# Optimization experiments

Measured on AMD Instinct MI355X. Metric: run time of the kernel, lower is better.

## Reference

```python
import jax, jax.numpy as jnp
import numpy as np

V = 64                 # |Sigma|
IN_DIM = V + 2         # Sigma + '(' + ')'
OUT_DIM = V + 1        # Sigma + <del>/<end>
H = 512
B = 256
SX = 34                # max proto length 32 + 2 boundaries
SY = 34
BIG_NEG = -1000000000.0


def _one_hot_seq(key, S, batch):
    # '(' at pos 0, L random symbols, ')' at pos L+1, zero padding after
    kl, ks = jax.random.split(key)
    lengths = jax.random.randint(kl, (batch,), 4, S - 1)        # L in [4, S-2]
    syms = jax.random.randint(ks, (S, batch), 0, V)
    pos = jnp.arange(S)[:, None]
    tok = jnp.where(pos == 0, V, jnp.where(pos == lengths[None, :] + 1, V + 1, syms))
    oh = jax.nn.one_hot(tok, IN_DIM, dtype=jnp.float32)
    valid = (pos <= lengths[None, :] + 1).astype(jnp.float32)
    return oh * valid[:, :, None]


def setup_inputs() -> dict:
    key = jax.random.key(0)
    ks = jax.random.split(key, 14)

    def p(k, shape, scale):
        return jax.random.uniform(k, shape, jnp.float32, -scale, scale)

    s = 1.0 / float(np.sqrt(H))
    s2 = 1.0 / float(np.sqrt(2 * H))
    return {
        "sources": _one_hot_seq(ks[0], SX, B),
        "targets": _one_hot_seq(ks[1], SY, B),
        # bidirectional prior LSTM (input IN_DIM -> hidden H, fwd + rev)
        "Wih_f": p(ks[2], (4 * H, IN_DIM), s), "Whh_f": p(ks[3], (4 * H, H), s), "b_f": p(ks[4], (4 * H,), s),
        "Wih_r": p(ks[5], (4 * H, IN_DIM), s), "Whh_r": p(ks[6], (4 * H, H), s), "b_r": p(ks[7], (4 * H,), s),
        # modern LSTM (input IN_DIM -> hidden 2H)
        "Wih_m": p(ks[8], (8 * H, IN_DIM), s2), "Whh_m": p(ks[9], (8 * H, 2 * H), s2), "b_m": p(ks[10], (8 * H,), s2),
        # heads: Linear(2H -> OUT_DIM) + LogSoftmax
        "W_sub": p(ks[11], (OUT_DIM, 2 * H), s2), "b_sub": jnp.zeros((OUT_DIM,), jnp.float32),
        "W_ins": p(ks[12], (OUT_DIM, 2 * H), s2), "b_ins": jnp.zeros((OUT_DIM,), jnp.float32),
    }


def _lstm(x, Wih, Whh, b, hid):
    # torch gate order: i, f, g, o
    bsz = x.shape[1]
    def step(carry, xt):
        h, c = carry
        g = xt @ Wih.T + h @ Whh.T + b
        i, f, gg, o = jnp.split(g, 4, axis=-1)
        c = jax.nn.sigmoid(f) * c + jax.nn.sigmoid(i) * jnp.tanh(gg)
        h = jax.nn.sigmoid(o) * jnp.tanh(c)
        return (h, c), h
    init = (jnp.zeros((bsz, hid), x.dtype), jnp.zeros((bsz, hid), x.dtype))
    _, hs = jax.lax.scan(step, init, x)
    return hs  # [S, B, hid]


def _forward(sources, targets, Wih_f, Whh_f, b_f, Wih_r, Whh_r, b_r,
             Wih_m, Whh_m, b_m, W_sub, b_sub, W_ins, b_ins):
    x_fwd = _lstm(sources, Wih_f, Whh_f, b_f, H)
    x_bwd = _lstm(sources[::-1], Wih_r, Whh_r, b_r, H)[::-1]
    x_emb = jnp.concatenate([x_fwd, x_bwd], axis=-1)   # [SX, B, 2H]
    y_emb = _lstm(targets, Wih_m, Whh_m, b_m, 2 * H)    # [SY, B, 2H]

    # head(x_emb[i] + y_emb[j]) decomposes since Linear is affine
    def pair_logprobs(W, bb):
        lx = jnp.einsum('ibh,oh->ibo', x_emb, W)              # [SX, B, O]
        ly = jnp.einsum('jbh,oh->jbo', y_emb, W) + bb         # [SY, B, O]
        return jax.nn.log_softmax(lx[:, None] + ly[None, :], axis=-1)  # [SX, SY, B, O]

    sub_log = pair_logprobs(W_sub, b_sub)
    ins_log = pair_logprobs(W_ins, b_ins)

    # cell (i, j, b) is computed iff x[i] and y[j] are real (non-padding) one-hots, j <= max_cognat_length
    x_any = sources.sum(-1) > 0                                # [SX, B]
    y_any = targets.sum(-1) > 0                                # [SY, B]
    j_ok = jnp.arange(SY) < SY - 1
    valid = x_any[:, None, :] & (y_any & j_ok[:, None])[None, :, :]   # [SX, SY, B]

    end = jnp.where(valid, ins_log[..., V], BIG_NEG)           # insProbs[V_SIZE]
    dlt = jnp.where(valid, sub_log[..., V], BIG_NEG)           # subProbs[V_SIZE]

    y_next = jnp.pad(targets[1:], ((0, 1), (0, 0), (0, 0)))    # y[j+1], [SY, B, IN_DIM]
    ins_ok = valid & (y_next[..., IN_DIM - 1] == 0)[None]      # not bool(y[j+1, V_SIZE+1])
    ins_val = jnp.einsum('ijbv,jbv->ijb', ins_log[..., :V], y_next[..., :V])
    sub_val = jnp.einsum('ijbv,jbv->ijb', sub_log[..., :V], y_next[..., :V])

    # stacked cached probs: [ins, sub, end, del], each [SX, SY, B]
    return jnp.stack([
        jnp.where(ins_ok, ins_val, BIG_NEG),
        jnp.where(ins_ok, sub_val, BIG_NEG),
        end,
        dlt,
    ])


def reference(sources, targets, Wih_f, Whh_f, b_f, Wih_r, Whh_r, b_r,
              Wih_m, Whh_m, b_m, W_sub, b_sub, W_ins, b_ins):
    return _forward(sources, targets, Wih_f, Whh_f, b_f, Wih_r, Whh_r, b_r,
                    Wih_m, Whh_m, b_m, W_sub, b_sub, W_ins, b_ins)
```

## Files before the change

### kernel.cpp

```cpp
#include <hip/hip_runtime.h>

typedef __attribute__((ext_vector_type(4))) float f32x4;
typedef unsigned char u8;
typedef unsigned long long u64t;

#define BIG_NEG -1000000000.0f

static constexpr int B_  = 256;
static constexpr int SX_ = 34;
static constexpr int SY_ = 34;
static constexpr int IND = 66;
static constexpr int OP_ = 80;

__device__ __forceinline__ f32x4 mfma_fp8(long a, long b, f32x4 c) {
  return __builtin_amdgcn_mfma_f32_16x16x32_fp8_fp8(a, b, c, 0, 0, 0);
}
__device__ __forceinline__ float sigm(float x)  { return 1.0f / (1.0f + __expf(-x)); }
__device__ __forceinline__ float tanhx(float x) { return 2.0f * sigm(2.0f * x) - 1.0f; }
template <bool HI>
__device__ __forceinline__ unsigned pk2(float a, float b, unsigned old) {
  return __builtin_amdgcn_cvt_pk_fp8_f32(a, b, (int)old, HI);
}

__global__ void decode_tokens(const float* __restrict__ src,
                              const float* __restrict__ tgt,
                              int* __restrict__ tok_x, int* __restrict__ tok_y) {
  int idx = blockIdx.x * 256 + threadIdx.x;
  const int half = SX_ * B_;
  if (idx >= 2 * half) return;
  const float* base = (idx < half) ? src : tgt;
  int* outp         = (idx < half) ? tok_x : tok_y;
  int k = (idx < half) ? idx : idx - half;
  const float* p = base + (size_t)k * IND;
  int tok = -1;
  for (int v = 0; v < IND; ++v) if (p[v] > 0.5f) tok = v;
  outp[k] = tok;
}

__global__ void conv_fp8_all(const float* __restrict__ Wf, const float* __restrict__ Wr,
                             const float* __restrict__ Wm,
                             u8* __restrict__ of, u8* __restrict__ orr, u8* __restrict__ om) {
  const int F4 = 2048 * 512 / 4;
  const int M4 = 4096 * 1024 / 4;
  int i = blockIdx.x * 256 + threadIdx.x;
  int stride = gridDim.x * 256;
  for (; i < 2 * F4 + M4; i += stride) {
    const float* src; unsigned* dst; int k;
    if (i < F4)          { src = Wf; dst = (unsigned*)of;  k = i; }
    else if (i < 2 * F4) { src = Wr; dst = (unsigned*)orr; k = i - F4; }
    else                 { src = Wm; dst = (unsigned*)om;  k = i - 2 * F4; }
    float4 f = ((const float4*)src)[k];
    unsigned w = pk2<false>(f.x, f.y, 0);
    w = pk2<true>(f.z, f.w, w);
    dst[k] = w;
  }
}

__global__ __launch_bounds__(256) void build_E_all(
    const float* __restrict__ Wf, const float* __restrict__ bf,
    const float* __restrict__ Wr, const float* __restrict__ br,
    const float* __restrict__ Wm, const float* __restrict__ bm,
    float* __restrict__ Ef, float* __restrict__ Er, float* __restrict__ Em) {
  __shared__ float tile[64 * 67];
  int tb = blockIdx.x;
  const float* W; const float* bias; float* E; int H4; int n0;
  if (tb < 32)      { W = Wf; bias = bf; E = Ef; H4 = 2048; n0 = tb * 64; }
  else if (tb < 64) { W = Wr; bias = br; E = Er; H4 = 2048; n0 = (tb - 32) * 64; }
  else              { W = Wm; bias = bm; E = Em; H4 = 4096; n0 = (tb - 64) * 64; }
  const float* src = W + (size_t)n0 * IND;
  for (int i = threadIdx.x; i < 64 * IND; i += 256) {
    int n = i / IND, v = i - n * IND;
    tile[n * 67 + v] = src[i];
  }
  __syncthreads();
  int lane = threadIdx.x & 63, w = threadIdx.x >> 6;
  float bl = bias[n0 + lane];
  for (int v = w; v < 67; v += 4) {
    float val = (v < 66 ? tile[lane * 67 + v] : 0.f) + bl;
    E[(size_t)v * H4 + n0 + lane] = val;
  }
}

__global__ void pad_head_w(const float* __restrict__ Wsub, const float* __restrict__ Wins,
                           u8* __restrict__ Wcat) {
  int widx = blockIdx.x * 256 + threadIdx.x;
  if (widx >= 160 * 256) return;
  int row = widx >> 8;
  int wc  = widx & 255;
  int srow = row < 80 ? row : row - 80;
  const float* W = row < 80 ? Wsub : Wins;
  float f0 = 0.f, f1 = 0.f, f2 = 0.f, f3 = 0.f;
  if (srow < 65) {
    const float* p = W + (size_t)srow * 1024 + wc * 4;
    f0 = p[0]; f1 = p[1]; f2 = p[2]; f3 = p[3];
  }
  unsigned w = pk2<false>(f0, f1, 0);
  w = pk2<true>(f2, f3, w);
  ((unsigned*)Wcat)[widx] = w;
}

template <int HH, int NS>
__device__ __forceinline__ void run_lstm(
    const u8* __restrict__ w8, const float* __restrict__ E,
    bool revr, u8* __restrict__ hall, int b0, int h0,
    unsigned* __restrict__ flags, int dom0, int myid,
    u8* __restrict__ alds, u8* __restrict__ hT, const u8* __restrict__ tok_small) {
  const int tid = threadIdx.x;
  const int lane = tid & 63, w = tid >> 6;
  const int lo = lane & 15, q = lane >> 4;
  constexpr int AST = HH + 8;
  constexpr int U8C = HH / 8;
  constexpr int USH = (HH == 1024) ? 7 : 6;
  constexpr int NI  = (32 * U8C) / 256;
  constexpr int NK  = HH / 32;
  const int hh = lo & 7;
  const bool hi = (lo >= 8);
  const int hu_e = h0 + w * 8 + hh;

  long breg0[NK], breg1[NK];
  {
    const u8* brow0 = w8 + (size_t)((lo >> 3) * HH + hu_e) * HH + q * 8;
    const u8* brow1 = w8 + (size_t)((2 + (lo >> 3)) * HH + hu_e) * HH + q * 8;
#pragma unroll
    for (int kk = 0; kk < NK; ++kk) {
      breg0[kk] = *(const long*)(brow0 + kk * 32);
      breg1[kk] = *(const long*)(brow1 + kk * 32);
    }
  }
  float creg[4] = {0.f, 0.f, 0.f, 0.f};

  for (int t = 0; t < 34; ++t) {
    const u8* hsrc = hall + (size_t)t * (256 * HH);
    u64t tmp[NI];
#pragma unroll
    for (int ii = 0; ii < NI; ++ii) {
      int idx = tid + ii * 256;
      tmp[ii] = __hip_atomic_load(
          (const u64t*)(hsrc + (size_t)(b0 + (idx >> USH)) * HH + (idx & (U8C - 1)) * 8),
          __ATOMIC_RELAXED, __HIP_MEMORY_SCOPE_AGENT);
    }
#pragma unroll
    for (int ii = 0; ii < NI; ++ii) {
      int idx = tid + ii * 256;
      *(u64t*)&alds[(idx >> USH) * AST + (idx & (U8C - 1)) * 8] = tmp[ii];
    }
    __syncthreads();

    f32x4 acc[2][2];
#pragma unroll
    for (int mt = 0; mt < 2; ++mt) {
      acc[mt][0] = (f32x4){0.f, 0.f, 0.f, 0.f};
      acc[mt][1] = (f32x4){0.f, 0.f, 0.f, 0.f};
    }
    const u8* a0p = alds + lo * AST + q * 8;
    const u8* a1p = alds + (16 + lo) * AST + q * 8;
#pragma unroll
    for (int kk = 0; kk < NK; ++kk) {
      long a0 = *(const long*)(a0p + kk * 32);
      long a1 = *(const long*)(a1p + kk * 32);
      acc[0][0] = mfma_fp8(a0, breg0[kk], acc[0][0]);
      acc[0][1] = mfma_fp8(a0, breg1[kk], acc[0][1]);
      acc[1][0] = mfma_fp8(a1, breg0[kk], acc[1][0]);
      acc[1][1] = mfma_fp8(a1, breg1[kk], acc[1][1]);
    }

    int tpos = revr ? 33 - t : t;
    const u8* tkp = tok_small + tpos * 32;
#pragma unroll
    for (int mt = 0; mt < 2; ++mt) {
      f32x4 t0 = acc[mt][0], t1 = acc[mt][1];
      f32x4 p0, p1;
#pragma unroll
      for (int c2 = 0; c2 < 4; ++c2) {
        p0[c2] = __shfl_xor(t0[c2], 8, 64);
        p1[c2] = __shfl_xor(t1[c2], 8, 64);
      }
#pragma unroll
      for (int rr = 0; rr < 2; ++rr) {
        int r = (hi ? 2 : 0) + rr;
        float iv = hi ? p0[r] : t0[r];
        float fv = hi ? t0[r] : p0[r];
        float gv = hi ? p1[r] : t1[r];
        float ov = hi ? t1[r] : p1[r];
        int m = mt * 16 + q * 4 + r;
        int v = tkp[m];
        const float* e = E + (size_t)v * (4 * HH) + hu_e;
        iv += e[0]; fv += e[HH]; gv += e[2 * HH]; ov += e[3 * HH];
        float cold = creg[mt * 2 + rr];
        float cn = sigm(fv) * cold + sigm(iv) * tanhx(gv);
        float hn = sigm(ov) * tanhx(cn);
        creg[mt * 2 + rr] = cn;
        hT[m * 32 + w * 8 + hh] = (u8)(pk2<false>(hn, hn, 0) & 0xffu);
      }
    }
    __syncthreads();

    {
      int m = tid >> 3, cc = tid & 7;
      unsigned val = *(const unsigned*)&hT[m * 32 + cc * 4];
      u8* hdst = hall + (size_t)(t + 1) * (256 * HH);
      __hip_atomic_store((unsigned*)(hdst + (size_t)(b0 + m) * HH + h0 + cc * 4),
                         val, __ATOMIC_RELAXED, __HIP_MEMORY_SCOPE_AGENT);
    }

    if (t < 33) {
      __asm__ volatile("s_waitcnt vmcnt(0)" ::: "memory");
      __syncthreads();
      unsigned tgt = (unsigned)(t + 1);
      if (tid == 0)
        __hip_atomic_store(&flags[(dom0 + myid) * 32], tgt,
                           __ATOMIC_RELAXED, __HIP_MEMORY_SCOPE_AGENT);
      if (tid < NS) {
        int spin = 0;
        for (;;) {
          unsigned v = __hip_atomic_load(&flags[(dom0 + tid) * 32],
                                         __ATOMIC_RELAXED, __HIP_MEMORY_SCOPE_AGENT);
          if (__ballot(v < tgt) == 0) break;
          __builtin_amdgcn_s_sleep(1);
          if (++spin > (1 << 17)) break;
        }
      }
      __syncthreads();
    }
  }
}

__global__ __launch_bounds__(256, 2) void lstm_persist(
    const int* __restrict__ tok_x, const int* __restrict__ tok_y,
    const float* __restrict__ E_f, const u8* __restrict__ w8_f,
    const float* __restrict__ E_r, const u8* __restrict__ w8_r,
    const float* __restrict__ E_m, const u8* __restrict__ w8_m,
    u8* __restrict__ fwd_all, u8* __restrict__ rev_all, u8* __restrict__ y_all,
    unsigned* __restrict__ flags) {
  __shared__ u8 alds[32 * 1032];
  __shared__ u8 hT[32 * 32];
  __shared__ u8 tok_small[34 * 32];

  const int b = blockIdx.x;
  int role, c, s;
  if (b < 256)      { role = 2; c = b >> 5; s = b & 31; }
  else if (b < 384) { int l = b - 256; role = 0; c = l >> 4; s = l & 15; }
  else              { int l = b - 384; role = 1; c = l >> 4; s = l & 15; }

  const float* E  = role == 0 ? E_f  : role == 1 ? E_r  : E_m;
  const u8*    w8 = role == 0 ? w8_f : role == 1 ? w8_r : w8_m;
  u8* hall        = role == 0 ? fwd_all : role == 1 ? rev_all : y_all;
  const int* tokg = (role == 2) ? tok_y : tok_x;
  const int b0 = c * 32;
  const int h0 = s * 32;
  const int dom0 = (role == 2) ? c * 32 : (role == 0) ? 256 + c * 16 : 384 + c * 16;

  for (int i = threadIdx.x; i < 34 * 32; i += 256) {
    int t2 = i >> 5, m = i & 31;
    int tk = tokg[t2 * 256 + b0 + m];
    tok_small[i] = (u8)(tk < 0 ? 66 : tk);
  }
  __syncthreads();

  if (role == 2)
    run_lstm<1024, 32>(w8, E, false, hall, b0, h0, flags, dom0, s, alds, hT, tok_small);
  else
    run_lstm<512, 16>(w8, E, role == 1, hall, b0, h0, flags, dom0, s, alds, hT, tok_small);
}

__global__ __launch_bounds__(256, 1) void head_kernel(
    const u8* __restrict__ fwd_all, const u8* __restrict__ rev_all,
    const u8* __restrict__ y_all, const u8* __restrict__ Wcat,
    const float* __restrict__ b_sub, const float* __restrict__ b_ins,
    float* __restrict__ lx_sub, float* __restrict__ lx_ins,
    float* __restrict__ ly_sub, float* __restrict__ ly_ins) {
  __shared__ u8 wq[160 * 264];
  const int lane = threadIdx.x & 63, wave = threadIdx.x >> 6;
  const int lo = lane & 15, q = lane >> 4;
  int blk = blockIdx.x;
  bool yside = (blk >= 68);
  int mb = yside ? blk - 68 : blk;
  int ij = mb >> 1;
  int bbase = (mb & 1) * 128;

  f32x4 acc[2][10];
#pragma unroll
  for (int mt = 0; mt < 2; ++mt)
#pragma unroll
    for (int nn = 0; nn < 10; ++nn) acc[mt][nn] = (f32x4){0.f,0.f,0.f,0.f};

  for (int qk = 0; qk < 4; ++qk) {
    long aA[2][8];
#pragma unroll
    for (int mt = 0; mt < 2; ++mt) {
      int row = bbase + wave * 32 + mt * 16 + lo;
      const u8* ab;
      if (yside)
        ab = y_all + ((size_t)(ij + 1) * 256 + row) * 1024 + qk * 256 + q * 8;
      else if (qk < 2)
        ab = fwd_all + ((size_t)(ij + 1) * 256 + row) * 512 + qk * 256 + q * 8;
      else
        ab = rev_all + ((size_t)(34 - ij) * 256 + row) * 512 + (qk - 2) * 256 + q * 8;
#pragma unroll
      for (int ki = 0; ki < 8; ++ki) aA[mt][ki] = *(const long*)(ab + ki * 32);
    }

    for (int c8 = threadIdx.x; c8 < 160 * 32; c8 += 256) {
      int row = c8 >> 5, col = (c8 & 31) << 3;
      *(long*)&wq[row * 264 + col] =
          *(const long*)&Wcat[(size_t)row * 1024 + qk * 256 + col];
    }
    __syncthreads();

#pragma unroll
    for (int ki = 0; ki < 8; ++ki) {
#pragma unroll
      for (int nn = 0; nn < 10; ++nn) {
        long bf = *(const long*)&wq[(nn * 16 + lo) * 264 + ki * 32 + q * 8];
        acc[0][nn] = mfma_fp8(aA[0][ki], bf, acc[0][nn]);
        acc[1][nn] = mfma_fp8(aA[1][ki], bf, acc[1][nn]);
      }
    }
    __syncthreads();
  }

#pragma unroll
  for (int mt = 0; mt < 2; ++mt) {
#pragma unroll
    for (int nn = 0; nn < 10; ++nn) {
      bool is_sub = (nn < 5);
      int n = (is_sub ? nn : nn - 5) * 16 + lo;
      float bias = 0.0f;
      if (yside && n < 65) bias = is_sub ? b_sub[n] : b_ins[n];
      float* dst = yside ? (is_sub ? ly_sub : ly_ins) : (is_sub ? lx_sub : lx_ins);
#pragma unroll
      for (int r = 0; r < 4; ++r) {
        int b = bbase + wave * 32 + mt * 16 + q * 4 + r;
        dst[((size_t)ij * 256 + b) * OP_ + n] = acc[mt][nn][r] + bias;
      }
    }
  }
}

__device__ __forceinline__ void lse_regs(const float4* __restrict__ X,
                                         const float* __restrict__ py, int sym,
                                         float& logZ, float& v64, float& vs) {
  const float4* py4 = (const float4*)py;
  float4 Y[17];
#pragma unroll
  for (int q = 0; q < 17; ++q) Y[q] = py4[q];
  float mm = -3.4e38f;
#pragma unroll
  for (int q = 0; q < 17; ++q) {
    float vx[4] = {X[q].x + Y[q].x, X[q].y + Y[q].y, X[q].z + Y[q].z, X[q].w + Y[q].w};
#pragma unroll
    for (int c = 0; c < 4; ++c) {
      int o = q * 4 + c;
      if (o < 65) mm = fmaxf(mm, vx[c]);
    }
  }
  float ss = 0.f, vsl = 0.f, vend = 0.f;
#pragma unroll
  for (int q = 0; q < 17; ++q) {
    float vx[4] = {X[q].x + Y[q].x, X[q].y + Y[q].y, X[q].z + Y[q].z, X[q].w + Y[q].w};
#pragma unroll
    for (int c = 0; c < 4; ++c) {
      int o = q * 4 + c;
      if (o < 65) {
        ss += __expf(vx[c] - mm);
        if (o == 64) vend = vx[c];
        if (o == sym) vsl = vx[c];
      }
    }
  }
  logZ = mm + __logf(ss);
  v64 = vend;
  vs = vsl;
}

__global__ __launch_bounds__(256, 1) void pair_kernel(
    const int* __restrict__ tok_x, const int* __restrict__ tok_y,
    const float* __restrict__ lx_sub, const float* __restrict__ lx_ins,
    const float* __restrict__ ly_sub, const float* __restrict__ ly_ins,
    float* __restrict__ out) {
  const int i = blockIdx.x >> 2;
  const int bc = blockIdx.x & 3;
  const int jq = threadIdx.x >> 6;
  const int bl = threadIdx.x & 63;
  const int b = bc * 64 + bl;
  const size_t CH = (size_t)SX_ * SY_ * B_;

  float4 Xs[17], Xi[17];
  {
    const float4* ps = (const float4*)(lx_sub + ((size_t)i * 256 + b) * OP_);
    const float4* pi = (const float4*)(lx_ins + ((size_t)i * 256 + b) * OP_);
#pragma unroll
    for (int q = 0; q < 17; ++q) { Xs[q] = ps[q]; Xi[q] = pi[q]; }
  }
  int tx = tok_x[i * 256 + b];

  for (int j = jq; j < 34; j += 4) {
    size_t obase = ((size_t)i * SY_ + j) * 256 + b;
    bool dead = (j == SY_ - 1) || (tx < 0);
    if (!dead) {
      int ty = tok_y[j * 256 + b];
      if (ty < 0) dead = true;
    }
    if (dead) {
      out[obase] = BIG_NEG;
      out[CH + obase] = BIG_NEG;
      out[2 * CH + obase] = BIG_NEG;
      out[3 * CH + obase] = BIG_NEG;
      continue;
    }
    int tn = tok_y[(j + 1) * 256 + b];
    bool ins_ok = (tn != 65);
    int sym = (tn >= 0 && tn < 64) ? tn : -1;

    float logZs, v64s, vss;
    lse_regs(Xs, ly_sub + ((size_t)j * 256 + b) * OP_, sym, logZs, v64s, vss);
    float dlt = v64s - logZs;
    float sub_val = (sym >= 0) ? (vss - logZs) : 0.0f;

    float logZi, v64i, vsi;
    lse_regs(Xi, ly_ins + ((size_t)j * 256 + b) * OP_, sym, logZi, v64i, vsi);
    float endv = v64i - logZi;
    float ins_val = (sym >= 0) ? (vsi - logZi) : 0.0f;

    out[obase]          = ins_ok ? ins_val : BIG_NEG;
    out[CH + obase]     = ins_ok ? sub_val : BIG_NEG;
    out[2 * CH + obase] = endv;
    out[3 * CH + obase] = dlt;
  }
}

extern "C" void kernel_launch(void* const* d_in, const int* in_sizes, int n_in,
                              void* d_out, int out_size, void* d_ws, size_t ws_size,
                              hipStream_t stream) {
  const float* sources = (const float*)d_in[0];
  const float* targets = (const float*)d_in[1];
  const float* Wih_f = (const float*)d_in[2];
  const float* Whh_f = (const float*)d_in[3];
  const float* b_f   = (const float*)d_in[4];
  const float* Wih_r = (const float*)d_in[5];
  const float* Whh_r = (const float*)d_in[6];
  const float* b_r   = (const float*)d_in[7];
  const float* Wih_m = (const float*)d_in[8];
  const float* Whh_m = (const float*)d_in[9];
  const float* b_m   = (const float*)d_in[10];
  const float* W_sub = (const float*)d_in[11];
  const float* b_sub = (const float*)d_in[12];
  const float* W_ins = (const float*)d_in[13];
  const float* b_ins = (const float*)d_in[14];
  float* out = (float*)d_out;

  char* w = (char*)d_ws;
  constexpr size_t FLAG_SZ = 512 * 32 * 4;
  constexpr size_t TOK_SZ  = (size_t)SX_ * B_ * 4;
  constexpr size_t WCAT_SZ = (size_t)160 * 1024;
  constexpr size_t W8F_SZ  = (size_t)2048 * 512;
  constexpr size_t W8M_SZ  = (size_t)4096 * 1024;
  constexpr size_t EF_SZ   = (size_t)67 * 2048 * 4;
  constexpr size_t EM_SZ   = (size_t)67 * 4096 * 4;
  constexpr size_t LX_SZ   = (size_t)SX_ * B_ * OP_ * 4;
  constexpr size_t HF_SZ   = (size_t)35 * B_ * 512;
  constexpr size_t HM_SZ   = (size_t)35 * B_ * 1024;

  size_t off = 0;
  unsigned* flags = (unsigned*)(w + off); off += FLAG_SZ;
  int*  tok_x   = (int*)(w + off);  off += TOK_SZ;
  int*  tok_y   = (int*)(w + off);  off += TOK_SZ;
  off = (off + 255) & ~(size_t)255;
  u8*   Wcat    = (u8*)(w + off);   off += WCAT_SZ;
  u8*   w8_f    = (u8*)(w + off);   off += W8F_SZ;
  u8*   w8_r    = (u8*)(w + off);   off += W8F_SZ;
  u8*   w8_m    = (u8*)(w + off);   off += W8M_SZ;
  float* E_f    = (float*)(w + off); off += EF_SZ;
  float* E_r    = (float*)(w + off); off += EF_SZ;
  float* E_m    = (float*)(w + off); off += EM_SZ;
  float* lx_sub = (float*)(w + off); off += LX_SZ;
  float* lx_ins = (float*)(w + off); off += LX_SZ;
  float* ly_sub = (float*)(w + off); off += LX_SZ;
  float* ly_ins = (float*)(w + off); off += LX_SZ;
  u8* fwd_all   = (u8*)(w + off);   off += HF_SZ;
  u8* rev_all   = (u8*)(w + off);   off += HF_SZ;
  u8* y_all     = (u8*)(w + off);   off += HM_SZ;
  (void)ws_size; (void)in_sizes; (void)n_in; (void)out_size;

  (void)hipMemsetAsync(flags, 0, FLAG_SZ, stream);
  (void)hipMemsetAsync(fwd_all, 0, (size_t)B_ * 512, stream);
  (void)hipMemsetAsync(rev_all, 0, (size_t)B_ * 512, stream);
  (void)hipMemsetAsync(y_all,   0, (size_t)B_ * 1024, stream);

  decode_tokens<<<(2 * SX_ * B_ + 255) / 256, 256, 0, stream>>>(sources, targets, tok_x, tok_y);
  pad_head_w<<<160, 256, 0, stream>>>(W_sub, W_ins, Wcat);
  conv_fp8_all<<<3072, 256, 0, stream>>>(Whh_f, Whh_r, Whh_m, w8_f, w8_r, w8_m);
  build_E_all<<<128, 256, 0, stream>>>(Wih_f, b_f, Wih_r, b_r, Wih_m, b_m, E_f, E_r, E_m);

  lstm_persist<<<512, 256, 0, stream>>>(
      tok_x, tok_y,
      E_f, w8_f,
      E_r, w8_r,
      E_m, w8_m,
      fwd_all, rev_all, y_all, flags);

  head_kernel<<<136, 256, 0, stream>>>(fwd_all, rev_all, y_all, Wcat,
                                       b_sub, b_ins, lx_sub, lx_ins, ly_sub, ly_ins);

  pair_kernel<<<136, 256, 0, stream>>>(tok_x, tok_y, lx_sub, lx_ins,
                                       ly_sub, ly_ins, out);
}
```

Baseline: 370.6 us.

## Fuse prep kernels, skip zero-state step, double head/pair grid parallelism

Merges the four preprocessing kernels into one prep_all launch with block-range dispatch and removes three memsets by skipping the recurrent matmul at t=0, where h is zero. Halves the per-block work in head_kernel (64 rows per block, 272 blocks) and splits pair_kernel by head (sub vs ins) across 272 blocks, each doing one log-sum-exp per cell. This targets launch overhead and low occupancy in the tail kernels. The cost is more redundant loads of the shared weight tiles and of tokens in the split blocks.

```diff
diff --git a/kernel.cpp b/kernel.cpp
--- a/kernel.cpp
+++ b/kernel.cpp
@@ -22,81 +22,80 @@
   return __builtin_amdgcn_cvt_pk_fp8_f32(a, b, (int)old, HI);
 }
 
-__global__ void decode_tokens(const float* __restrict__ src,
-                              const float* __restrict__ tgt,
-                              int* __restrict__ tok_x, int* __restrict__ tok_y) {
-  int idx = blockIdx.x * 256 + threadIdx.x;
-  const int half = SX_ * B_;
-  if (idx >= 2 * half) return;
-  const float* base = (idx < half) ? src : tgt;
-  int* outp         = (idx < half) ? tok_x : tok_y;
-  int k = (idx < half) ? idx : idx - half;
-  const float* p = base + (size_t)k * IND;
-  int tok = -1;
-  for (int v = 0; v < IND; ++v) if (p[v] > 0.5f) tok = v;
-  outp[k] = tok;
-}
-
-__global__ void conv_fp8_all(const float* __restrict__ Wf, const float* __restrict__ Wr,
-                             const float* __restrict__ Wm,
-                             u8* __restrict__ of, u8* __restrict__ orr, u8* __restrict__ om) {
-  const int F4 = 2048 * 512 / 4;
-  const int M4 = 4096 * 1024 / 4;
-  int i = blockIdx.x * 256 + threadIdx.x;
-  int stride = gridDim.x * 256;
-  for (; i < 2 * F4 + M4; i += stride) {
-    const float* src; unsigned* dst; int k;
-    if (i < F4)          { src = Wf; dst = (unsigned*)of;  k = i; }
-    else if (i < 2 * F4) { src = Wr; dst = (unsigned*)orr; k = i - F4; }
-    else                 { src = Wm; dst = (unsigned*)om;  k = i - 2 * F4; }
-    float4 f = ((const float4*)src)[k];
-    unsigned w = pk2<false>(f.x, f.y, 0);
-    w = pk2<true>(f.z, f.w, w);
-    dst[k] = w;
-  }
-}
-
-__global__ __launch_bounds__(256) void build_E_all(
-    const float* __restrict__ Wf, const float* __restrict__ bf,
-    const float* __restrict__ Wr, const float* __restrict__ br,
-    const float* __restrict__ Wm, const float* __restrict__ bm,
-    float* __restrict__ Ef, float* __restrict__ Er, float* __restrict__ Em) {
+__global__ __launch_bounds__(256) void prep_all(
+    const float* __restrict__ src, const float* __restrict__ tgt,
+    int* __restrict__ tok_x, int* __restrict__ tok_y,
+    const float* __restrict__ Wsub, const float* __restrict__ Wins,
+    u8* __restrict__ Wcat,
+    const float* __restrict__ Wihf, const float* __restrict__ bf,
+    const float* __restrict__ Wihr, const float* __restrict__ br,
+    const float* __restrict__ Wihm, const float* __restrict__ bm,
+    float* __restrict__ Ef, float* __restrict__ Er, float* __restrict__ Em,
+    const float* __restrict__ Whf, const float* __restrict__ Whr,
+    const float* __restrict__ Whm,
+    u8* __restrict__ w8f, u8* __restrict__ w8r, u8* __restrict__ w8m) {
   __shared__ float tile[64 * 67];
-  int tb = blockIdx.x;
-  const float* W; const float* bias; float* E; int H4; int n0;
-  if (tb < 32)      { W = Wf; bias = bf; E = Ef; H4 = 2048; n0 = tb * 64; }
-  else if (tb < 64) { W = Wr; bias = br; E = Er; H4 = 2048; n0 = (tb - 32) * 64; }
-  else              { W = Wm; bias = bm; E = Em; H4 = 4096; n0 = (tb - 64) * 64; }
-  const float* src = W + (size_t)n0 * IND;
-  for (int i = threadIdx.x; i < 64 * IND; i += 256) {
-    int n = i / IND, v = i - n * IND;
-    tile[n * 67 + v] = src[i];
-  }
-  __syncthreads();
-  int lane = threadIdx.x & 63, w = threadIdx.x >> 6;
-  float bl = bias[n0 + lane];
-  for (int v = w; v < 67; v += 4) {
-    float val = (v < 66 ? tile[lane * 67 + v] : 0.f) + bl;
-    E[(size_t)v * H4 + n0 + lane] = val;
-  }
-}
-
-__global__ void pad_head_w(const float* __restrict__ Wsub, const float* __restrict__ Wins,
-                           u8* __restrict__ Wcat) {
-  int widx = blockIdx.x * 256 + threadIdx.x;
-  if (widx >= 160 * 256) return;
-  int row = widx >> 8;
-  int wc  = widx & 255;
-  int srow = row < 80 ? row : row - 80;
-  const float* W = row < 80 ? Wsub : Wins;
-  float f0 = 0.f, f1 = 0.f, f2 = 0.f, f3 = 0.f;
-  if (srow < 65) {
-    const float* p = W + (size_t)srow * 1024 + wc * 4;
-    f0 = p[0]; f1 = p[1]; f2 = p[2]; f3 = p[3];
-  }
-  unsigned w = pk2<false>(f0, f1, 0);
-  w = pk2<true>(f2, f3, w);
-  ((unsigned*)Wcat)[widx] = w;
+  const int blk = blockIdx.x;
+  const int tid = threadIdx.x;
+
+  if (blk < 68) {
+    int idx = blk * 256 + tid;
+    const int half = SX_ * B_;
+    const float* base = (idx < half) ? src : tgt;
+    int* outp         = (idx < half) ? tok_x : tok_y;
+    int k = (idx < half) ? idx : idx - half;
+    const float* p = base + (size_t)k * IND;
+    int tok = -1;
+    for (int v = 0; v < IND; ++v) if (p[v] > 0.5f) tok = v;
+    outp[k] = tok;
+  } else if (blk < 228) {
+    int widx = (blk - 68) * 256 + tid;
+    int row = widx >> 8;
+    int wc  = widx & 255;
+    int srow = row < 80 ? row : row - 80;
+    const float* W = row < 80 ? Wsub : Wins;
+    float f0 = 0.f, f1 = 0.f, f2 = 0.f, f3 = 0.f;
+    if (srow < 65) {
+      const float* p = W + (size_t)srow * 1024 + wc * 4;
+      f0 = p[0]; f1 = p[1]; f2 = p[2]; f3 = p[3];
+    }
+    unsigned w = pk2<false>(f0, f1, 0);
+    w = pk2<true>(f2, f3, w);
+    ((unsigned*)Wcat)[widx] = w;
+  } else if (blk < 356) {
+    int tb = blk - 228;
+    const float* W; const float* bias; float* E; int H4; int n0;
+    if (tb < 32)      { W = Wihf; bias = bf; E = Ef; H4 = 2048; n0 = tb * 64; }
+    else if (tb < 64) { W = Wihr; bias = br; E = Er; H4 = 2048; n0 = (tb - 32) * 64; }
+    else              { W = Wihm; bias = bm; E = Em; H4 = 4096; n0 = (tb - 64) * 64; }
+    const float* s2 = W + (size_t)n0 * IND;
+    for (int i = tid; i < 64 * IND; i += 256) {
+      int n = i / IND, v = i - n * IND;
+      tile[n * 67 + v] = s2[i];
+    }
+    __syncthreads();
+    int lane = tid & 63, w2 = tid >> 6;
+    float bl = bias[n0 + lane];
+    for (int v = w2; v < 67; v += 4) {
+      float val = (v < 66 ? tile[lane * 67 + v] : 0.f) + bl;
+      E[(size_t)v * H4 + n0 + lane] = val;
+    }
+  } else {
+    const int F4 = 2048 * 512 / 4;
+    const int M4 = 4096 * 1024 / 4;
+    int i = (blk - 356) * 256 + tid;
+    int stride = 3072 * 256;
+    for (; i < 2 * F4 + M4; i += stride) {
+      const float* s3; unsigned* dst; int k;
+      if (i < F4)          { s3 = Whf; dst = (unsigned*)w8f; k = i; }
+      else if (i < 2 * F4) { s3 = Whr; dst = (unsigned*)w8r; k = i - F4; }
+      else                 { s3 = Whm; dst = (unsigned*)w8m; k = i - 2 * F4; }
+      float4 f = ((const float4*)s3)[k];
+      unsigned w3 = pk2<false>(f.x, f.y, 0);
+      w3 = pk2<true>(f.z, f.w, w3);
+      dst[k] = w3;
+    }
+  }
 }
 
 template <int HH, int NS>
@@ -130,38 +129,41 @@
   float creg[4] = {0.f, 0.f, 0.f, 0.f};
 
   for (int t = 0; t < 34; ++t) {
-    const u8* hsrc = hall + (size_t)t * (256 * HH);
-    u64t tmp[NI];
-#pragma unroll
-    for (int ii = 0; ii < NI; ++ii) {
-      int idx = tid + ii * 256;
-      tmp[ii] = __hip_atomic_load(
-          (const u64t*)(hsrc + (size_t)(b0 + (idx >> USH)) * HH + (idx & (U8C - 1)) * 8),
-          __ATOMIC_RELAXED, __HIP_MEMORY_SCOPE_AGENT);
-    }
-#pragma unroll
-    for (int ii = 0; ii < NI; ++ii) {
-      int idx = tid + ii * 256;
-      *(u64t*)&alds[(idx >> USH) * AST + (idx & (U8C - 1)) * 8] = tmp[ii];
-    }
-    __syncthreads();
-
     f32x4 acc[2][2];
 #pragma unroll
     for (int mt = 0; mt < 2; ++mt) {
       acc[mt][0] = (f32x4){0.f, 0.f, 0.f, 0.f};
       acc[mt][1] = (f32x4){0.f, 0.f, 0.f, 0.f};
     }
-    const u8* a0p = alds + lo * AST + q * 8;
-    const u8* a1p = alds + (16 + lo) * AST + q * 8;
-#pragma unroll
-    for (int kk = 0; kk < NK; ++kk) {
-      long a0 = *(const long*)(a0p + kk * 32);
-      long a1 = *(const long*)(a1p + kk * 32);
-      acc[0][0] = mfma_fp8(a0, breg0[kk], acc[0][0]);
-      acc[0][1] = mfma_fp8(a0, breg1[kk], acc[0][1]);
-      acc[1][0] = mfma_fp8(a1, breg0[kk], acc[1][0]);
-      acc[1][1] = mfma_fp8(a1, breg1[kk], acc[1][1]);
+
+    if (t > 0) {
+      const u8* hsrc = hall + (size_t)t * (256 * HH);
+      u64t tmp[NI];
+#pragma unroll
+      for (int ii = 0; ii < NI; ++ii) {
+        int idx = tid + ii * 256;
+        tmp[ii] = __hip_atomic_load(
+            (const u64t*)(hsrc + (size_t)(b0 + (idx >> USH)) * HH + (idx & (U8C - 1)) * 8),
+            __ATOMIC_RELAXED, __HIP_MEMORY_SCOPE_AGENT);
+      }
+#pragma unroll
+      for (int ii = 0; ii < NI; ++ii) {
+        int idx = tid + ii * 256;
+        *(u64t*)&alds[(idx >> USH) * AST + (idx & (U8C - 1)) * 8] = tmp[ii];
+      }
+      __syncthreads();
+
+      const u8* a0p = alds + lo * AST + q * 8;
+      const u8* a1p = alds + (16 + lo) * AST + q * 8;
+#pragma unroll
+      for (int kk = 0; kk < NK; ++kk) {
+        long a0 = *(const long*)(a0p + kk * 32);
+        long a1 = *(const long*)(a1p + kk * 32);
+        acc[0][0] = mfma_fp8(a0, breg0[kk], acc[0][0]);
+        acc[0][1] = mfma_fp8(a0, breg1[kk], acc[0][1]);
+        acc[1][0] = mfma_fp8(a1, breg0[kk], acc[1][0]);
+        acc[1][1] = mfma_fp8(a1, breg1[kk], acc[1][1]);
+      }
     }
 
     int tpos = revr ? 33 - t : t;
@@ -273,22 +275,19 @@
   const int lane = threadIdx.x & 63, wave = threadIdx.x >> 6;
   const int lo = lane & 15, q = lane >> 4;
   int blk = blockIdx.x;
-  bool yside = (blk >= 68);
-  int mb = yside ? blk - 68 : blk;
-  int ij = mb >> 1;
-  int bbase = (mb & 1) * 128;
-
-  f32x4 acc[2][10];
-#pragma unroll
-  for (int mt = 0; mt < 2; ++mt)
-#pragma unroll
-    for (int nn = 0; nn < 10; ++nn) acc[mt][nn] = (f32x4){0.f,0.f,0.f,0.f};
+  bool yside = (blk >= 136);
+  int mb = yside ? blk - 136 : blk;
+  int ij = mb >> 2;
+  int bbase = (mb & 3) * 64;
+
+  f32x4 acc[10];
+#pragma unroll
+  for (int nn = 0; nn < 10; ++nn) acc[nn] = (f32x4){0.f,0.f,0.f,0.f};
 
   for (int qk = 0; qk < 4; ++qk) {
-    long aA[2][8];
-#pragma unroll
-    for (int mt = 0; mt < 2; ++mt) {
-      int row = bbase + wave * 32 + mt * 16 + lo;
+    long aA[8];
+    {
+      int row = bbase + wave * 16 + lo;
       const u8* ab;
       if (yside)
         ab = y_all + ((size_t)(ij + 1) * 256 + row) * 1024 + qk * 256 + q * 8;
@@ -297,7 +296,7 @@
       else
         ab = rev_all + ((size_t)(34 - ij) * 256 + row) * 512 + (qk - 2) * 256 + q * 8;
 #pragma unroll
-      for (int ki = 0; ki < 8; ++ki) aA[mt][ki] = *(const long*)(ab + ki * 32);
+      for (int ki = 0; ki < 8; ++ki) aA[ki] = *(const long*)(ab + ki * 32);
     }
 
     for (int c8 = threadIdx.x; c8 < 160 * 32; c8 += 256) {
@@ -312,64 +311,51 @@
 #pragma unroll
       for (int nn = 0; nn < 10; ++nn) {
         long bf = *(const long*)&wq[(nn * 16 + lo) * 264 + ki * 32 + q * 8];
-        acc[0][nn] = mfma_fp8(aA[0][ki], bf, acc[0][nn]);
-        acc[1][nn] = mfma_fp8(aA[1][ki], bf, acc[1][nn]);
+        acc[nn] = mfma_fp8(aA[ki], bf, acc[nn]);
       }
     }
     __syncthreads();
   }
 
 #pragma unroll
-  for (int mt = 0; mt < 2; ++mt) {
-#pragma unroll
-    for (int nn = 0; nn < 10; ++nn) {
-      bool is_sub = (nn < 5);
-      int n = (is_sub ? nn : nn - 5) * 16 + lo;
-      float bias = 0.0f;
-      if (yside && n < 65) bias = is_sub ? b_sub[n] : b_ins[n];
-      float* dst = yside ? (is_sub ? ly_sub : ly_ins) : (is_sub ? lx_sub : lx_ins);
-#pragma unroll
-      for (int r = 0; r < 4; ++r) {
-        int b = bbase + wave * 32 + mt * 16 + q * 4 + r;
-        dst[((size_t)ij * 256 + b) * OP_ + n] = acc[mt][nn][r] + bias;
-      }
-    }
-  }
-}
-
-__device__ __forceinline__ void lse_regs(const float4* __restrict__ X,
-                                         const float* __restrict__ py, int sym,
-                                         float& logZ, float& v64, float& vs) {
+  for (int nn = 0; nn < 10; ++nn) {
+    bool is_sub = (nn < 5);
+    int n = (is_sub ? nn : nn - 5) * 16 + lo;
+    float bias = 0.0f;
+    if (yside && n < 65) bias = is_sub ? b_sub[n] : b_ins[n];
+    float* dst = yside ? (is_sub ? ly_sub : ly_ins) : (is_sub ? lx_sub : lx_ins);
+#pragma unroll
+    for (int r = 0; r < 4; ++r) {
+      int b = bbase + wave * 16 + q * 4 + r;
+      dst[((size_t)ij * 256 + b) * OP_ + n] = acc[nn][r] + bias;
+    }
+  }
+}
+
+__device__ __forceinline__ void lse_one(const float4* __restrict__ X,
+                                        const float* __restrict__ py, int sym,
+                                        float& logZ, float& v64, float& vs) {
+  float v[68];
   const float4* py4 = (const float4*)py;
-  float4 Y[17];
-#pragma unroll
-  for (int q = 0; q < 17; ++q) Y[q] = py4[q];
-  float mm = -3.4e38f;
 #pragma unroll
   for (int q = 0; q < 17; ++q) {
-    float vx[4] = {X[q].x + Y[q].x, X[q].y + Y[q].y, X[q].z + Y[q].z, X[q].w + Y[q].w};
-#pragma unroll
-    for (int c = 0; c < 4; ++c) {
-      int o = q * 4 + c;
-      if (o < 65) mm = fmaxf(mm, vx[c]);
-    }
-  }
-  float ss = 0.f, vsl = 0.f, vend = 0.f;
-#pragma unroll
-  for (int q = 0; q < 17; ++q) {
-    float vx[4] = {X[q].x + Y[q].x, X[q].y + Y[q].y, X[q].z + Y[q].z, X[q].w + Y[q].w};
-#pragma unroll
-    for (int c = 0; c < 4; ++c) {
-      int o = q * 4 + c;
-      if (o < 65) {
-        ss += __expf(vx[c] - mm);
-        if (o == 64) vend = vx[c];
-        if (o == sym) vsl = vx[c];
-      }
-    }
-  }
-  logZ = mm + __logf(ss);
-  v64 = vend;
+    float4 yb = py4[q];
+    v[4 * q + 0] = X[q].x + yb.x;
+    v[4 * q + 1] = X[q].y + yb.y;
+    v[4 * q + 2] = X[q].z + yb.z;
+    v[4 * q + 3] = X[q].w + yb.w;
+  }
+  float m = v[0];
+#pragma unroll
+  for (int o = 1; o < 65; ++o) m = fmaxf(m, v[o]);
+  float s = 0.0f, vsl = 0.0f;
+#pragma unroll
+  for (int o = 0; o < 65; ++o) {
+    s += __expf(v[o] - m);
+    if (o < 64) vsl = (o == sym) ? v[o] : vsl;
+  }
+  logZ = m + __logf(s);
+  v64 = v[64];
   vs = vsl;
 }
 
@@ -378,19 +364,24 @@
     const float* __restrict__ lx_sub, const float* __restrict__ lx_ins,
     const float* __restrict__ ly_sub, const float* __restrict__ ly_ins,
     float* __restrict__ out) {
-  const int i = blockIdx.x >> 2;
-  const int bc = blockIdx.x & 3;
+  const int hsel = blockIdx.x >= 136;
+  const int rem = hsel ? blockIdx.x - 136 : blockIdx.x;
+  const int i = rem >> 2;
+  const int bc = rem & 3;
   const int jq = threadIdx.x >> 6;
   const int bl = threadIdx.x & 63;
   const int b = bc * 64 + bl;
   const size_t CH = (size_t)SX_ * SY_ * B_;
-
-  float4 Xs[17], Xi[17];
+  const float* lx = hsel ? lx_ins : lx_sub;
+  const float* ly = hsel ? ly_ins : ly_sub;
+  float* outA = out + (hsel ? 0 : CH);
+  float* outB = out + (hsel ? 2 * CH : 3 * CH);
+
+  float4 X[17];
   {
-    const float4* ps = (const float4*)(lx_sub + ((size_t)i * 256 + b) * OP_);
-    const float4* pi = (const float4*)(lx_ins + ((size_t)i * 256 + b) * OP_);
-#pragma unroll
-    for (int q = 0; q < 17; ++q) { Xs[q] = ps[q]; Xi[q] = pi[q]; }
+    const float4* ps = (const float4*)(lx + ((size_t)i * 256 + b) * OP_);
+#pragma unroll
+    for (int q = 0; q < 17; ++q) X[q] = ps[q];
   }
   int tx = tok_x[i * 256 + b];
 
@@ -402,30 +393,20 @@
       if (ty < 0) dead = true;
     }
     if (dead) {
-      out[obase] = BIG_NEG;
-      out[CH + obase] = BIG_NEG;
-      out[2 * CH + obase] = BIG_NEG;
-      out[3 * CH + obase] = BIG_NEG;
+      outA[obase] = BIG_NEG;
+      outB[obase] = BIG_NEG;
       continue;
     }
     int tn = tok_y[(j + 1) * 256 + b];
     bool ins_ok = (tn != 65);
     int sym = (tn >= 0 && tn < 64) ? tn : -1;
 
-    float logZs, v64s, vss;
-    lse_regs(Xs, ly_sub + ((size_t)j * 256 + b) * OP_, sym, logZs, v64s, vss);
-    float dlt = v64s - logZs;
-    float sub_val = (sym >= 0) ? (vss - logZs) : 0.0f;
-
-    float logZi, v64i, vsi;
-    lse_regs(Xi, ly_ins + ((size_t)j * 256 + b) * OP_, sym, logZi, v64i, vsi);
-    float endv = v64i - logZi;
-    float ins_val = (sym >= 0) ? (vsi - logZi) : 0.0f;
-
-    out[obase]          = ins_ok ? ins_val : BIG_NEG;
-    out[CH + obase]     = ins_ok ? sub_val : BIG_NEG;
-    out[2 * CH + obase] = endv;
-    out[3 * CH + obase] = dlt;
+    float logZ, v64, vs;
+    lse_one(X, ly + ((size_t)j * 256 + b) * OP_, sym, logZ, v64, vs);
+    float valB = v64 - logZ;
+    float valA = (sym >= 0) ? (vs - logZ) : 0.0f;
+    outA[obase] = ins_ok ? valA : BIG_NEG;
+    outB[obase] = valB;
   }
 }
 
@@ -483,14 +464,12 @@
   (void)ws_size; (void)in_sizes; (void)n_in; (void)out_size;
 
   (void)hipMemsetAsync(flags, 0, FLAG_SZ, stream);
-  (void)hipMemsetAsync(fwd_all, 0, (size_t)B_ * 512, stream);
-  (void)hipMemsetAsync(rev_all, 0, (size_t)B_ * 512, stream);
-  (void)hipMemsetAsync(y_all,   0, (size_t)B_ * 1024, stream);
-
-  decode_tokens<<<(2 * SX_ * B_ + 255) / 256, 256, 0, stream>>>(sources, targets, tok_x, tok_y);
-  pad_head_w<<<160, 256, 0, stream>>>(W_sub, W_ins, Wcat);
-  conv_fp8_all<<<3072, 256, 0, stream>>>(Whh_f, Whh_r, Whh_m, w8_f, w8_r, w8_m);
-  build_E_all<<<128, 256, 0, stream>>>(Wih_f, b_f, Wih_r, b_r, Wih_m, b_m, E_f, E_r, E_m);
+
+  prep_all<<<3428, 256, 0, stream>>>(
+      sources, targets, tok_x, tok_y,
+      W_sub, W_ins, Wcat,
+      Wih_f, b_f, Wih_r, b_r, Wih_m, b_m, E_f, E_r, E_m,
+      Whh_f, Whh_r, Whh_m, w8_f, w8_r, w8_m);
 
   lstm_persist<<<512, 256, 0, stream>>>(
       tok_x, tok_y,
@@ -499,9 +478,9 @@
       E_m, w8_m,
       fwd_all, rev_all, y_all, flags);
 
-  head_kernel<<<136, 256, 0, stream>>>(fwd_all, rev_all, y_all, Wcat,
+  head_kernel<<<272, 256, 0, stream>>>(fwd_all, rev_all, y_all, Wcat,
                                        b_sub, b_ins, lx_sub, lx_ins, ly_sub, ly_ins);
 
-  pair_kernel<<<136, 256, 0, stream>>>(tok_x, tok_y, lx_sub, lx_ins,
+  pair_kernel<<<272, 256, 0, stream>>>(tok_x, tok_y, lx_sub, lx_ins,
                                        ly_sub, ly_ins, out);
 }
```

After: 339.3 us. 1.09x faster.
